# Kernel tuning notes

Hardware: AMD Instinct MI355X
Metric: run time of the kernel (lower is better)

## Reference

```python
import jax, jax.numpy as jnp
import numpy as np

N = 50000   # nodes
E = 600000  # edges
D = 128     # emb_dim
L = 3       # num_layers
G = 500     # graphs in batch
AV = 128    # atom feature vocab per column (9 columns)
BV = 8      # bond feature vocab per column (3 columns)


def setup_inputs() -> dict:
    key = jax.random.key(0)
    ks = jax.random.split(key, 16)
    r = lambda k, sh: jax.random.normal(k, sh, jnp.float32) * 0.02
    return dict(
        x=jax.random.randint(ks[0], (N, 9), 0, AV),
        edge_index=jax.random.randint(ks[1], (2, E), 0, N),
        edge_attr=jax.random.randint(ks[2], (E, 3), 0, BV),
        batch=(jnp.arange(N) * G) // N,  # sorted node->graph map, covers all G graphs
        atom_emb=r(ks[3], (9, AV, D)),
        bond_emb=r(ks[4], (L, 3, BV, D)),  # per-layer BondEncoder
        eps=jnp.zeros((L,), jnp.float32),
        conv_w1=r(ks[5], (L, D, 2 * D)), conv_b1=jnp.zeros((L, 2 * D), jnp.float32),
        conv_bn_g=jnp.ones((L, 2 * D), jnp.float32), conv_bn_b=jnp.zeros((L, 2 * D), jnp.float32),
        conv_w2=r(ks[6], (L, 2 * D, D)), conv_b2=jnp.zeros((L, D), jnp.float32),
        bn_g=jnp.ones((L, D), jnp.float32), bn_b=jnp.zeros((L, D), jnp.float32),
        vn_emb=jnp.zeros((1, D), jnp.float32),  # init constant 0, as in torch code
        vn_w1=r(ks[7], (L - 1, D, 2 * D)), vn_b1=jnp.zeros((L - 1, 2 * D), jnp.float32),
        vn_bn1_g=jnp.ones((L - 1, 2 * D), jnp.float32), vn_bn1_b=jnp.zeros((L - 1, 2 * D), jnp.float32),
        vn_w2=r(ks[8], (L - 1, 2 * D, D)), vn_b2=jnp.zeros((L - 1, D), jnp.float32),
        vn_bn2_g=jnp.ones((L - 1, D), jnp.float32), vn_bn2_b=jnp.zeros((L - 1, D), jnp.float32),
    )


def _bn(h, g, b):
    # BatchNorm1d, training-mode batch statistics (biased var), eps=1e-5
    mu = h.mean(0)
    var = h.var(0)
    return (h - mu) * jax.lax.rsqrt(var + 1e-5) * g + b


def reference(x, edge_index, edge_attr, batch, atom_emb, bond_emb, eps,
              conv_w1, conv_b1, conv_bn_g, conv_bn_b, conv_w2, conv_b2,
              bn_g, bn_b, vn_emb, vn_w1, vn_b1, vn_bn1_g, vn_bn1_b,
              vn_w2, vn_b2, vn_bn2_g, vn_bn2_b):
    src, dst = edge_index[0], edge_index[1]
    # AtomEncoder: sum of per-column embeddings -> [N, D]
    h = sum(atom_emb[i][x[:, i]] for i in range(9))
    vn = jnp.broadcast_to(vn_emb[0], (G, D))  # virtualnode_embedding(zeros(G))
    for l in range(L):
        h = h + vn[batch]                                   # virtual-node broadcast
        ee = sum(bond_emb[l, i][edge_attr[:, i]] for i in range(3))  # BondEncoder [E, D]
        msg = jax.nn.relu(h[src] + ee)                      # message: relu(x_j + edge_attr)
        agg = jax.ops.segment_sum(msg, dst, num_segments=N)  # aggr='add'
        t = (1.0 + eps[l]) * h + agg
        t = _bn(t @ conv_w1[l] + conv_b1[l], conv_bn_g[l], conv_bn_b[l])
        t = jax.nn.relu(t) @ conv_w2[l] + conv_b2[l]
        hn = _bn(t, bn_g[l], bn_b[l])                       # outer batch_norms[layer]
        if l < L - 1:
            hn = jax.nn.relu(hn)                            # relu before dropout (non-final)
            # virtual node update: global_add_pool(h_list[layer]) + vn -> MLP
            vt = jax.ops.segment_sum(h, batch, num_segments=G) + vn
            vt = jax.nn.relu(_bn(vt @ vn_w1[l] + vn_b1[l], vn_bn1_g[l], vn_bn1_b[l]))
            vn = jax.nn.relu(_bn(vt @ vn_w2[l] + vn_b2[l], vn_bn2_g[l], vn_bn2_b[l]))
        h = hn
    return h
```

## Files before the change

kernel.cpp:

```cpp
#include <hip/hip_runtime.h>

#define DEV __global__ __launch_bounds__(256)

constexpr int NN = 50000;
constexpr int NE = 600000;
constexpr int D  = 128;
constexpr int NG = 500;
constexpr int NL = 3;
constexpr int SCAN_B = 512;
constexpr int NBLK = (NN + SCAN_B - 1) / SCAN_B;

typedef __attribute__((ext_vector_type(8))) short bf16x8;
typedef __attribute__((ext_vector_type(4))) float f32x4;

__device__ inline ushort f2bf(float f) {
  unsigned u = __builtin_bit_cast(unsigned, f);
  unsigned r = u + 0x7FFFu + ((u >> 16) & 1u);
  return (ushort)(r >> 16);
}
__device__ inline float bf2f(ushort h) {
  unsigned u = ((unsigned)h) << 16;
  return __builtin_bit_cast(float, u);
}


DEV void k_atom(const int* __restrict__ x, const float* __restrict__ emb,
                const float* __restrict__ vne, float* __restrict__ hv) {
  int t = blockIdx.x * 256 + threadIdx.x;
  int n = t >> 5, c = (t & 31) * 4;
  if (n >= NN) return;
  float4 acc = *(const float4*)(vne + c);
  #pragma unroll
  for (int i = 0; i < 9; ++i) {
    int v = x[n * 9 + i];
    float4 e = *(const float4*)(emb + ((size_t)(i * 128 + v)) * D + c);
    acc.x += e.x; acc.y += e.y; acc.z += e.z; acc.w += e.w;
  }
  *(float4*)(hv + (size_t)n * D + c) = acc;
}

DEV void k_vninit(const float* __restrict__ src, float* __restrict__ vn) {
  int t = blockIdx.x * 256 + threadIdx.x;
  int g = t >> 5, c = (t & 31) * 4;
  if (g >= NG) return;
  *(float4*)(vn + (size_t)g * D + c) = *(const float4*)(src + c);
}

DEV void k_post(const float* __restrict__ z, const float* __restrict__ sum,
                const float* __restrict__ sq, const float* __restrict__ gam,
                const float* __restrict__ bet, float invM,
                const float* __restrict__ vnadd, const int* __restrict__ batch,
                float* __restrict__ dst, int M, int relu) {
  int t = blockIdx.x * 256 + threadIdx.x;
  int n = t >> 5, c = (t & 31) * 4;
  if (n >= M) return;
  f32x4 s = *(const f32x4*)(sum + c);
  f32x4 q = *(const f32x4*)(sq + c);
  f32x4 g = *(const f32x4*)(gam + c);
  f32x4 b = *(const f32x4*)(bet + c);
  f32x4 v = *(const f32x4*)(z + (size_t)n * 128 + c);
  f32x4 o;
  #pragma unroll
  for (int j = 0; j < 4; ++j) {
    float mu = s[j] * invM;
    float var = q[j] * invM - mu * mu;
    float sc = g[j] * rsqrtf(var + 1e-5f);
    float sh = b[j] - mu * sc;
    o[j] = fmaf(v[j], sc, sh);
    if (relu) o[j] = fmaxf(o[j], 0.f);
  }
  if (vnadd) {
    f32x4 a = *(const f32x4*)(vnadd + (size_t)batch[n] * 128 + c);
    #pragma unroll
    for (int j = 0; j < 4; ++j) o[j] += a[j];
  }
  *(f32x4*)(dst + (size_t)n * 128 + c) = o;
}


DEV void k_hist(const int* __restrict__ ei, int* __restrict__ cnt) {
  int e = blockIdx.x * 256 + threadIdx.x;
  if (e < NE) atomicAdd(&cnt[ei[NE + e]], 1);
}

__global__ __launch_bounds__(SCAN_B) void k_scan_a(const int* __restrict__ cnt,
                                                   int* __restrict__ rowptr,
                                                   int* __restrict__ bsum) {
  __shared__ int sh[SCAN_B];
  int i = blockIdx.x * SCAN_B + threadIdx.x;
  int v = (i < NN) ? cnt[i] : 0;
  sh[threadIdx.x] = v;
  __syncthreads();
  for (int off = 1; off < SCAN_B; off <<= 1) {
    int u = (threadIdx.x >= (unsigned)off) ? sh[threadIdx.x - off] : 0;
    __syncthreads();
    sh[threadIdx.x] += u;
    __syncthreads();
  }
  if (i < NN) rowptr[i + 1] = sh[threadIdx.x];
  if (threadIdx.x == SCAN_B - 1) bsum[blockIdx.x] = sh[SCAN_B - 1];
}

__global__ void k_scan_b(int* __restrict__ bsum, int nb) {
  if (threadIdx.x == 0 && blockIdx.x == 0) {
    int acc = 0;
    for (int i = 0; i < nb; ++i) { int v = bsum[i]; bsum[i] = acc; acc += v; }
  }
}

__global__ __launch_bounds__(SCAN_B) void k_scan_c(int* __restrict__ rowptr,
                                                   const int* __restrict__ bsum) {
  int i = blockIdx.x * SCAN_B + threadIdx.x;
  if (i < NN) rowptr[i + 1] += bsum[blockIdx.x];
  if (i == 0) rowptr[0] = 0;
}

DEV void k_fill(const int* __restrict__ ei, const int* __restrict__ eattr,
                int* __restrict__ cursor, unsigned* __restrict__ csr) {
  int e = blockIdx.x * 256 + threadIdx.x;
  if (e >= NE) return;
  int dn = ei[NE + e];
  int p = atomicAdd(&cursor[dn], 1);
  unsigned a0 = (unsigned)eattr[e * 3 + 0];
  unsigned a1 = (unsigned)eattr[e * 3 + 1];
  unsigned a2 = (unsigned)eattr[e * 3 + 2];
  csr[p] = (unsigned)ei[e] | (a0 << 17) | (a1 << 20) | (a2 << 23);
}


DEV void k_agg(const float* __restrict__ hv, const unsigned* __restrict__ csr,
               const int* __restrict__ rowptr, const float* __restrict__ bond,
               float* __restrict__ agg) {
  __shared__ float eb[3 * 8 * D];
  for (int i = threadIdx.x; i < 3 * 8 * D; i += 256) eb[i] = bond[i];
  __syncthreads();
  int wid = (blockIdx.x * 256 + threadIdx.x) >> 6;
  int lane = threadIdx.x & 63;
  if (wid >= NN) return;
  int d0 = lane * 2;
  float ax = 0.f, ay = 0.f;
  int p = rowptr[wid];
  const int p1 = rowptr[wid + 1];
  for (; p + 4 <= p1; p += 4) {
    unsigned pk[4];
    #pragma unroll
    for (int j = 0; j < 4; ++j) pk[j] = csr[p + j];
    float2 hvv[4];
    #pragma unroll
    for (int j = 0; j < 4; ++j)
      hvv[j] = *(const float2*)(hv + (size_t)(pk[j] & 0x1FFFF) * D + d0);
    #pragma unroll
    for (int j = 0; j < 4; ++j) {
      float2 e0 = *(const float2*)(eb + (((pk[j] >> 17) & 7u)) * D + d0);
      float2 e1 = *(const float2*)(eb + (8 + ((pk[j] >> 20) & 7u)) * D + d0);
      float2 e2 = *(const float2*)(eb + (16 + ((pk[j] >> 23) & 7u)) * D + d0);
      ax += fmaxf(hvv[j].x + e0.x + e1.x + e2.x, 0.f);
      ay += fmaxf(hvv[j].y + e0.y + e1.y + e2.y, 0.f);
    }
  }
  for (; p < p1; ++p) {
    unsigned pk = csr[p];
    float2 hvv = *(const float2*)(hv + (size_t)(pk & 0x1FFFF) * D + d0);
    float2 e0 = *(const float2*)(eb + (((pk >> 17) & 7u)) * D + d0);
    float2 e1 = *(const float2*)(eb + (8 + ((pk >> 20) & 7u)) * D + d0);
    float2 e2 = *(const float2*)(eb + (16 + ((pk >> 23) & 7u)) * D + d0);
    ax += fmaxf(hvv.x + e0.x + e1.x + e2.x, 0.f);
    ay += fmaxf(hvv.y + e0.y + e1.y + e2.y, 0.f);
  }
  *(float2*)(agg + (size_t)wid * D + d0) = make_float2(ax, ay);
}

__global__ __launch_bounds__(256) void k_cvtw(const float* __restrict__ src, int K,
                                              int lognc, ushort* __restrict__ th,
                                              ushort* __restrict__ tl) {
  int NC = 1 << lognc;
  size_t base = (size_t)blockIdx.y * K * NC;
  int i = blockIdx.x * 256 + threadIdx.x;
  if (i >= K * NC) return;
  int k = i >> lognc, c = i & (NC - 1);
  float v = src[base + i];
  ushort hi = f2bf(v);
  th[base + (size_t)c * K + k] = hi;
  tl[base + (size_t)c * K + k] = f2bf(v - bf2f(hi));
}

template <int AMODE, int COLS, int NT>
__global__ __launch_bounds__(NT) void k_mgemm(
    int M, int K, const float* __restrict__ A0, const float* __restrict__ A1,
    const float* __restrict__ epsp, const float* __restrict__ bnsum,
    const float* __restrict__ bnsq, const float* __restrict__ bngam,
    const float* __restrict__ bnbet, float invPrevM,
    const ushort* __restrict__ Wth, const ushort* __restrict__ Wtl,
    const float* __restrict__ bias, float* __restrict__ Y,
    float* __restrict__ colsum, float* __restrict__ colsq) {
  constexpr int NWC = COLS / 64;
  __shared__ __align__(16) ushort Ah[4][128][8];
  __shared__ __align__(16) ushort Al[4][128][8];
  __shared__ __align__(16) ushort Bh[4][COLS][8];
  __shared__ __align__(16) ushort Bl[4][COLS][8];
  __shared__ float bnsc[AMODE == 2 ? 256 : 1];
  __shared__ float bnsh[AMODE == 2 ? 256 : 1];
  const int tid = threadIdx.x;
  const int row0 = blockIdx.x * 128;
  const int lane = tid & 63, w = tid >> 6;
  const int wr = w / NWC, wc = w % NWC;
  const int kc = lane >> 4, lr = lane & 15;

  if (AMODE == 2) {
    for (int c = tid; c < K; c += NT) {
      float mu = bnsum[c] * invPrevM;
      float var = bnsq[c] * invPrevM - mu * mu;
      float sc = bngam[c] * rsqrtf(var + 1e-5f);
      bnsc[c] = sc;
      bnsh[c] = bnbet[c] - mu * sc;
    }
    __syncthreads();
  }

  float ef = 0.f;
  if (AMODE == 1) ef = 1.f + *epsp;
  f32x4 acc[4][4] = {};

  for (int k0 = 0; k0 < K; k0 += 32) {
    for (int i = tid; i < 512; i += NT) {
      const int c = i >> 7, r = i & 127;
      const int gk = k0 + c * 8;
      const int gr = row0 + r;
      float v[8];
      if (gr < M) {
        f32x4 a0 = *(const f32x4*)(A0 + (size_t)gr * K + gk);
        f32x4 a1 = *(const f32x4*)(A0 + (size_t)gr * K + gk + 4);
        if (AMODE == 1) {
          f32x4 g0 = *(const f32x4*)(A1 + (size_t)gr * K + gk);
          f32x4 g1 = *(const f32x4*)(A1 + (size_t)gr * K + gk + 4);
          #pragma unroll
          for (int j = 0; j < 4; ++j) {
            v[j] = fmaf(ef, a0[j], g0[j]);
            v[4 + j] = fmaf(ef, a1[j], g1[j]);
          }
        } else if (AMODE == 2) {
          f32x4 s0 = *(const f32x4*)&bnsc[gk];
          f32x4 s1 = *(const f32x4*)&bnsc[gk + 4];
          f32x4 t0 = *(const f32x4*)&bnsh[gk];
          f32x4 t1 = *(const f32x4*)&bnsh[gk + 4];
          #pragma unroll
          for (int j = 0; j < 4; ++j) {
            v[j] = fmaxf(fmaf(a0[j], s0[j], t0[j]), 0.f);
            v[4 + j] = fmaxf(fmaf(a1[j], s1[j], t1[j]), 0.f);
          }
        } else {
          #pragma unroll
          for (int j = 0; j < 4; ++j) { v[j] = a0[j]; v[4 + j] = a1[j]; }
        }
      } else {
        #pragma unroll
        for (int j = 0; j < 8; ++j) v[j] = 0.f;
      }
      alignas(16) ushort th[8], tl[8];
      #pragma unroll
      for (int j = 0; j < 8; ++j) {
        ushort hi = f2bf(v[j]);
        th[j] = hi;
        tl[j] = f2bf(v[j] - bf2f(hi));
      }
      *(uint4*)&Ah[c][r][0] = *(const uint4*)th;
      *(uint4*)&Al[c][r][0] = *(const uint4*)tl;
    }
    for (int i = tid; i < COLS * 4; i += NT) {
      const int c = i / COLS, r = i % COLS;
      const int gk = k0 + c * 8;
      *(uint4*)&Bh[c][r][0] = *(const uint4*)(Wth + (size_t)r * K + gk);
      *(uint4*)&Bl[c][r][0] = *(const uint4*)(Wtl + (size_t)r * K + gk);
    }
    __syncthreads();
    bf16x8 bhf[4], blf[4];
    #pragma unroll
    for (int fc = 0; fc < 4; ++fc) {
      bhf[fc] = *(const bf16x8*)&Bh[kc][wc * 64 + fc * 16 + lr][0];
      blf[fc] = *(const bf16x8*)&Bl[kc][wc * 64 + fc * 16 + lr][0];
    }
    #pragma unroll
    for (int fr = 0; fr < 4; ++fr) {
      bf16x8 ahf = *(const bf16x8*)&Ah[kc][wr * 64 + fr * 16 + lr][0];
      bf16x8 alf = *(const bf16x8*)&Al[kc][wr * 64 + fr * 16 + lr][0];
      #pragma unroll
      for (int fc = 0; fc < 4; ++fc) {
        acc[fr][fc] = __builtin_amdgcn_mfma_f32_16x16x32_bf16(ahf, bhf[fc], acc[fr][fc], 0, 0, 0);
        acc[fr][fc] = __builtin_amdgcn_mfma_f32_16x16x32_bf16(alf, bhf[fc], acc[fr][fc], 0, 0, 0);
        acc[fr][fc] = __builtin_amdgcn_mfma_f32_16x16x32_bf16(ahf, blf[fc], acc[fr][fc], 0, 0, 0);
      }
    }
    __syncthreads();
  }

  #pragma unroll
  for (int fc = 0; fc < 4; ++fc) {
    const int gc = wc * 64 + fc * 16 + lr;
    const float bb = bias[gc];
    float cs = 0.f, cq = 0.f;
    #pragma unroll
    for (int fr = 0; fr < 4; ++fr) {
      const int rb = row0 + wr * 64 + fr * 16 + kc * 4;
      #pragma unroll
      for (int rg = 0; rg < 4; ++rg) {
        int gr = rb + rg;
        if (gr < M) {
          float v = acc[fr][fc][rg] + bb;
          Y[(size_t)gr * COLS + gc] = v;
          cs += v;
          cq += v * v;
        }
      }
    }
    cs += __shfl_xor(cs, 16); cs += __shfl_xor(cs, 32);
    cq += __shfl_xor(cq, 16); cq += __shfl_xor(cq, 32);
    if (kc == 0) {
      atomicAdd(&colsum[gc], cs);
      atomicAdd(&colsq[gc], cq);
    }
  }
}


DEV void k_pool(const float* __restrict__ hv, const int* __restrict__ batch,
                const float* __restrict__ vn, float* __restrict__ vt) {
  int g = blockIdx.x;
  int lo = 0, hi = NN;
  while (lo < hi) { int mid = (lo + hi) >> 1; if (batch[mid] < g) lo = mid + 1; else hi = mid; }
  int s = lo;
  hi = NN;
  while (lo < hi) { int mid = (lo + hi) >> 1; if (batch[mid] < g + 1) lo = mid + 1; else hi = mid; }
  int e = lo;
  int ry = threadIdx.x >> 5, cx = threadIdx.x & 31;
  float4 acc = make_float4(0.f, 0.f, 0.f, 0.f);
  for (int n = s + ry; n < e; n += 8) {
    float4 v = *(const float4*)(hv + (size_t)n * D + cx * 4);
    acc.x += v.x; acc.y += v.y; acc.z += v.z; acc.w += v.w;
  }
  __shared__ float4 red[8][32];
  red[ry][cx] = acc;
  __syncthreads();
  for (int st = 4; st >= 1; st >>= 1) {
    if (ry < st) {
      float4 o = red[ry + st][cx];
      red[ry][cx].x += o.x; red[ry][cx].y += o.y;
      red[ry][cx].z += o.z; red[ry][cx].w += o.w;
    }
    __syncthreads();
  }
  if (ry == 0) {
    float4 v = red[0][cx];
    float4 b = *(const float4*)(vn + (size_t)g * D + cx * 4);
    v.x += b.x; v.y += b.y; v.z += b.z; v.w += b.w;
    *(float4*)(vt + (size_t)g * D + cx * 4) = v;
  }
}


extern "C" void kernel_launch(void* const* d_in, const int* in_sizes, int n_in,
                              void* d_out, int out_size, void* d_ws, size_t ws_size,
                              hipStream_t stream) {
  const int* x = (const int*)d_in[0];
  const int* ei = (const int*)d_in[1];
  const int* eattr = (const int*)d_in[2];
  const int* batch = (const int*)d_in[3];
  const float* atom_emb = (const float*)d_in[4];
  const float* bond_emb = (const float*)d_in[5];
  const float* eps = (const float*)d_in[6];
  const float* conv_w1 = (const float*)d_in[7];
  const float* conv_b1 = (const float*)d_in[8];
  const float* conv_bn_g = (const float*)d_in[9];
  const float* conv_bn_b = (const float*)d_in[10];
  const float* conv_w2 = (const float*)d_in[11];
  const float* conv_b2 = (const float*)d_in[12];
  const float* bn_g = (const float*)d_in[13];
  const float* bn_b = (const float*)d_in[14];
  const float* vn_emb = (const float*)d_in[15];
  const float* vn_w1 = (const float*)d_in[16];
  const float* vn_b1 = (const float*)d_in[17];
  const float* vn_bn1_g = (const float*)d_in[18];
  const float* vn_bn1_b = (const float*)d_in[19];
  const float* vn_w2 = (const float*)d_in[20];
  const float* vn_b2 = (const float*)d_in[21];
  const float* vn_bn2_g = (const float*)d_in[22];
  const float* vn_bn2_b = (const float*)d_in[23];
  float* out = (float*)d_out;

  char* w = (char*)d_ws;
  auto alloc = [&](size_t bytes) {
    char* p = w;
    w += (bytes + 255) & ~((size_t)255);
    return p;
  };
  float* h   = (float*)alloc((size_t)NN * D * 4);
  float* hv  = (float*)alloc((size_t)NN * D * 4);
  float* agg = (float*)alloc((size_t)NN * D * 4);
  float* y   = (float*)alloc((size_t)NN * 256 * 4);
  float* vn  = (float*)alloc((size_t)NG * D * 4);
  float* vt  = (float*)alloc((size_t)NG * D * 4);
  float* yv  = (float*)alloc((size_t)NG * 256 * 4);
  float* zv  = (float*)alloc((size_t)NG * D * 4);
  float* stats = (float*)alloc(16 * 512 * 4);
  auto SUM = [&](int slot) { return stats + slot * 512; };
  auto SQ  = [&](int slot) { return stats + slot * 512 + 256; };
  int* cnt = (int*)alloc((size_t)NN * 4);
  int* rowptr = (int*)alloc((size_t)(NN + 1) * 4);
  int* cursor = (int*)alloc((size_t)NN * 4);
  unsigned* csr = (unsigned*)alloc((size_t)NE * 4);
  int* bsum = (int*)alloc(128 * 4);
  ushort* wt1h = (ushort*)alloc((size_t)NL * 256 * 128 * 2);
  ushort* wt1l = (ushort*)alloc((size_t)NL * 256 * 128 * 2);
  ushort* wt2h = (ushort*)alloc((size_t)NL * 128 * 256 * 2);
  ushort* wt2l = (ushort*)alloc((size_t)NL * 128 * 256 * 2);
  ushort* vw1h = (ushort*)alloc((size_t)2 * 256 * 128 * 2);
  ushort* vw1l = (ushort*)alloc((size_t)2 * 256 * 128 * 2);
  ushort* vw2h = (ushort*)alloc((size_t)2 * 128 * 256 * 2);
  ushort* vw2l = (ushort*)alloc((size_t)2 * 128 * 256 * 2);

  hipMemsetAsync(stats, 0, 16 * 512 * 4, stream);

  k_cvtw<<<dim3(128, NL), 256, 0, stream>>>(conv_w1, 128, 8, wt1h, wt1l);
  k_cvtw<<<dim3(128, NL), 256, 0, stream>>>(conv_w2, 256, 7, wt2h, wt2l);
  k_cvtw<<<dim3(128, 2), 256, 0, stream>>>(vn_w1, 128, 8, vw1h, vw1l);
  k_cvtw<<<dim3(128, 2), 256, 0, stream>>>(vn_w2, 256, 7, vw2h, vw2l);

  k_atom<<<(NN * 32 + 255) / 256, 256, 0, stream>>>(x, atom_emb, vn_emb, hv);
  k_vninit<<<(NG * 32 + 255) / 256, 256, 0, stream>>>(vn_emb, vn);

  hipMemsetAsync(cnt, 0, (size_t)NN * 4, stream);
  k_hist<<<(NE + 255) / 256, 256, 0, stream>>>(ei, cnt);
  k_scan_a<<<NBLK, SCAN_B, 0, stream>>>(cnt, rowptr, bsum);
  k_scan_b<<<1, 64, 0, stream>>>(bsum, NBLK);
  k_scan_c<<<NBLK, SCAN_B, 0, stream>>>(rowptr, bsum);
  hipMemcpyAsync(cursor, rowptr, (size_t)NN * 4, hipMemcpyDeviceToDevice, stream);
  k_fill<<<(NE + 255) / 256, 256, 0, stream>>>(ei, eattr, cursor, csr);

  const int gx = (NN + 127) / 128;
  const int gv = (NG + 127) / 128;
  for (int l = 0; l < NL; ++l) {
    const int sc1 = l, sc2 = 3 + l, sv1 = 6 + l, sv2 = 8 + l;
    k_agg<<<(NN * 64 + 255) / 256, 256, 0, stream>>>(
        hv, csr, rowptr, bond_emb + (size_t)l * 3 * 8 * D, agg);

    k_mgemm<1, 256, 512><<<gx, 512, 0, stream>>>(
        NN, 128, hv, agg, eps + l, nullptr, nullptr, nullptr, nullptr, 0.f,
        wt1h + (size_t)l * 256 * 128, wt1l + (size_t)l * 256 * 128,
        conv_b1 + l * 256, y, SUM(sc1), SQ(sc1));
    k_mgemm<2, 128, 256><<<gx, 256, 0, stream>>>(
        NN, 256, y, nullptr, nullptr, SUM(sc1), SQ(sc1),
        conv_bn_g + l * 256, conv_bn_b + l * 256, 1.f / NN,
        wt2h + (size_t)l * 128 * 256, wt2l + (size_t)l * 128 * 256,
        conv_b2 + l * 128, h, SUM(sc2), SQ(sc2));

    if (l < NL - 1) {
      k_pool<<<NG, 256, 0, stream>>>(hv, batch, vn, vt);
      k_mgemm<0, 256, 512><<<gv, 512, 0, stream>>>(
          NG, 128, vt, nullptr, nullptr, nullptr, nullptr, nullptr, nullptr, 0.f,
          vw1h + (size_t)l * 256 * 128, vw1l + (size_t)l * 256 * 128,
          vn_b1 + l * 256, yv, SUM(sv1), SQ(sv1));
      k_mgemm<2, 128, 256><<<gv, 256, 0, stream>>>(
          NG, 256, yv, nullptr, nullptr, SUM(sv1), SQ(sv1),
          vn_bn1_g + l * 256, vn_bn1_b + l * 256, 1.f / NG,
          vw2h + (size_t)l * 128 * 256, vw2l + (size_t)l * 128 * 256,
          vn_b2 + l * 128, zv, SUM(sv2), SQ(sv2));
      k_post<<<(NG * 32 + 255) / 256, 256, 0, stream>>>(
          zv, SUM(sv2), SQ(sv2), vn_bn2_g + l * 128, vn_bn2_b + l * 128,
          1.f / NG, nullptr, nullptr, vn, NG, 1);
      k_post<<<(NN * 32 + 255) / 256, 256, 0, stream>>>(
          h, SUM(sc2), SQ(sc2), bn_g + l * 128, bn_b + l * 128,
          1.f / NN, vn, batch, hv, NN, 1);
    } else {
      k_post<<<(NN * 32 + 255) / 256, 256, 0, stream>>>(
          h, SUM(sc2), SQ(sc2), bn_g + l * 128, bn_b + l * 128,
          1.f / NN, nullptr, nullptr, out, NN, 0);
    }
  }
}
```

Before: 874.8 us.

## Fuse eps-combine and bf16 split into aggregation; replace stat atomics with block partials

The aggregation kernel now adds (1+eps)*h itself and writes the result pre-split into bf16 hi/lo arrays. The first GEMM loads these directly instead of reading two fp32 tensors and converting them. Column sum and sum-of-squares for batch norm are first reduced across waves in shared memory. For the large GEMMs each block then writes per-block partials that a small reduction kernel sums, replacing global atomics. This cuts GEMM input traffic and atomic contention, at the cost of two extra kernel launches per layer and a serial loop over about 391 blocks in the reduction.

```diff
diff --git a/kernel.cpp b/kernel.cpp
--- a/kernel.cpp
+++ b/kernel.cpp
@@ -130,7 +130,8 @@
 
 DEV void k_agg(const float* __restrict__ hv, const unsigned* __restrict__ csr,
                const int* __restrict__ rowptr, const float* __restrict__ bond,
-               float* __restrict__ agg) {
+               const float* __restrict__ epsp, unsigned* __restrict__ Ahi,
+               unsigned* __restrict__ Alo) {
   __shared__ float eb[3 * 8 * D];
   for (int i = threadIdx.x; i < 3 * 8 * D; i += 256) eb[i] = bond[i];
   __syncthreads();
@@ -167,7 +168,14 @@
     ax += fmaxf(hvv.x + e0.x + e1.x + e2.x, 0.f);
     ay += fmaxf(hvv.y + e0.y + e1.y + e2.y, 0.f);
   }
-  *(float2*)(agg + (size_t)wid * D + d0) = make_float2(ax, ay);
+  float2 hvo = *(const float2*)(hv + (size_t)wid * D + d0);
+  float ef = 1.f + epsp[0];
+  float a0 = fmaf(ef, hvo.x, ax);
+  float a1 = fmaf(ef, hvo.y, ay);
+  ushort h0 = f2bf(a0), h1 = f2bf(a1);
+  ushort l0 = f2bf(a0 - bf2f(h0)), l1 = f2bf(a1 - bf2f(h1));
+  Ahi[(size_t)wid * 64 + lane] = (unsigned)h0 | ((unsigned)h1 << 16);
+  Alo[(size_t)wid * 64 + lane] = (unsigned)l0 | ((unsigned)l1 << 16);
 }
 
 __global__ __launch_bounds__(256) void k_cvtw(const float* __restrict__ src, int K,
@@ -184,15 +192,16 @@
   tl[base + (size_t)c * K + k] = f2bf(v - bf2f(hi));
 }
 
-template <int AMODE, int COLS, int NT>
+template <int AMODE, int COLS, int NT, bool ATOMIC>
 __global__ __launch_bounds__(NT) void k_mgemm(
-    int M, int K, const float* __restrict__ A0, const float* __restrict__ A1,
-    const float* __restrict__ epsp, const float* __restrict__ bnsum,
+    int M, int K, const float* __restrict__ A0, const ushort* __restrict__ Ath,
+    const ushort* __restrict__ Atl, const float* __restrict__ bnsum,
     const float* __restrict__ bnsq, const float* __restrict__ bngam,
     const float* __restrict__ bnbet, float invPrevM,
     const ushort* __restrict__ Wth, const ushort* __restrict__ Wtl,
     const float* __restrict__ bias, float* __restrict__ Y,
-    float* __restrict__ colsum, float* __restrict__ colsq) {
+    float* __restrict__ colsum, float* __restrict__ colsq,
+    float* __restrict__ partial) {
   constexpr int NWC = COLS / 64;
   __shared__ __align__(16) ushort Ah[4][128][8];
   __shared__ __align__(16) ushort Al[4][128][8];
@@ -217,8 +226,6 @@
     __syncthreads();
   }
 
-  float ef = 0.f;
-  if (AMODE == 1) ef = 1.f + *epsp;
   f32x4 acc[4][4] = {};
 
   for (int k0 = 0; k0 < K; k0 += 32) {
@@ -226,45 +233,47 @@
       const int c = i >> 7, r = i & 127;
       const int gk = k0 + c * 8;
       const int gr = row0 + r;
-      float v[8];
-      if (gr < M) {
-        f32x4 a0 = *(const f32x4*)(A0 + (size_t)gr * K + gk);
-        f32x4 a1 = *(const f32x4*)(A0 + (size_t)gr * K + gk + 4);
-        if (AMODE == 1) {
-          f32x4 g0 = *(const f32x4*)(A1 + (size_t)gr * K + gk);
-          f32x4 g1 = *(const f32x4*)(A1 + (size_t)gr * K + gk + 4);
-          #pragma unroll
-          for (int j = 0; j < 4; ++j) {
-            v[j] = fmaf(ef, a0[j], g0[j]);
-            v[4 + j] = fmaf(ef, a1[j], g1[j]);
-          }
-        } else if (AMODE == 2) {
-          f32x4 s0 = *(const f32x4*)&bnsc[gk];
-          f32x4 s1 = *(const f32x4*)&bnsc[gk + 4];
-          f32x4 t0 = *(const f32x4*)&bnsh[gk];
-          f32x4 t1 = *(const f32x4*)&bnsh[gk + 4];
-          #pragma unroll
-          for (int j = 0; j < 4; ++j) {
-            v[j] = fmaxf(fmaf(a0[j], s0[j], t0[j]), 0.f);
-            v[4 + j] = fmaxf(fmaf(a1[j], s1[j], t1[j]), 0.f);
+      if (AMODE == 3) {
+        uint4 vh = make_uint4(0, 0, 0, 0), vl = make_uint4(0, 0, 0, 0);
+        if (gr < M) {
+          vh = *(const uint4*)(Ath + (size_t)gr * K + gk);
+          vl = *(const uint4*)(Atl + (size_t)gr * K + gk);
+        }
+        *(uint4*)&Ah[c][r][0] = vh;
+        *(uint4*)&Al[c][r][0] = vl;
+      } else {
+        float v[8];
+        if (gr < M) {
+          f32x4 a0 = *(const f32x4*)(A0 + (size_t)gr * K + gk);
+          f32x4 a1 = *(const f32x4*)(A0 + (size_t)gr * K + gk + 4);
+          if (AMODE == 2) {
+            f32x4 s0 = *(const f32x4*)&bnsc[gk];
+            f32x4 s1 = *(const f32x4*)&bnsc[gk + 4];
+            f32x4 t0 = *(const f32x4*)&bnsh[gk];
+            f32x4 t1 = *(const f32x4*)&bnsh[gk + 4];
+            #pragma unroll
+            for (int j = 0; j < 4; ++j) {
+              v[j] = fmaxf(fmaf(a0[j], s0[j], t0[j]), 0.f);
+              v[4 + j] = fmaxf(fmaf(a1[j], s1[j], t1[j]), 0.f);
+            }
+          } else {
+            #pragma unroll
+            for (int j = 0; j < 4; ++j) { v[j] = a0[j]; v[4 + j] = a1[j]; }
           }
         } else {
           #pragma unroll
-          for (int j = 0; j < 4; ++j) { v[j] = a0[j]; v[4 + j] = a1[j]; }
+          for (int j = 0; j < 8; ++j) v[j] = 0.f;
         }
-      } else {
+        alignas(16) ushort th[8], tl[8];
         #pragma unroll
-        for (int j = 0; j < 8; ++j) v[j] = 0.f;
+        for (int j = 0; j < 8; ++j) {
+          ushort hi = f2bf(v[j]);
+          th[j] = hi;
+          tl[j] = f2bf(v[j] - bf2f(hi));
+        }
+        *(uint4*)&Ah[c][r][0] = *(const uint4*)th;
+        *(uint4*)&Al[c][r][0] = *(const uint4*)tl;
       }
-      alignas(16) ushort th[8], tl[8];
-      #pragma unroll
-      for (int j = 0; j < 8; ++j) {
-        ushort hi = f2bf(v[j]);
-        th[j] = hi;
-        tl[j] = f2bf(v[j] - bf2f(hi));
-      }
-      *(uint4*)&Ah[c][r][0] = *(const uint4*)th;
-      *(uint4*)&Al[c][r][0] = *(const uint4*)tl;
     }
     for (int i = tid; i < COLS * 4; i += NT) {
       const int c = i / COLS, r = i % COLS;
@@ -293,6 +302,8 @@
     __syncthreads();
   }
 
+  float* sred = reinterpret_cast<float*>(&Ah[0][0][0]);
+  float* qred = sred + 2 * COLS;
   #pragma unroll
   for (int fc = 0; fc < 4; ++fc) {
     const int gc = wc * 64 + fc * 16 + lr;
@@ -315,10 +326,33 @@
     cs += __shfl_xor(cs, 16); cs += __shfl_xor(cs, 32);
     cq += __shfl_xor(cq, 16); cq += __shfl_xor(cq, 32);
     if (kc == 0) {
-      atomicAdd(&colsum[gc], cs);
-      atomicAdd(&colsq[gc], cq);
-    }
-  }
+      sred[wr * COLS + gc] = cs;
+      qred[wr * COLS + gc] = cq;
+    }
+  }
+  __syncthreads();
+  for (int c = tid; c < COLS; c += NT) {
+    float s = sred[c] + sred[COLS + c];
+    float q = qred[c] + qred[COLS + c];
+    if (ATOMIC) {
+      atomicAdd(&colsum[c], s);
+      atomicAdd(&colsq[c], q);
+    } else {
+      partial[(size_t)blockIdx.x * 2 * COLS + c] = s;
+      partial[(size_t)blockIdx.x * 2 * COLS + COLS + c] = q;
+    }
+  }
+}
+
+__global__ __launch_bounds__(256) void k_red(const float* __restrict__ part, int nb,
+                                             int width, float* __restrict__ outSum,
+                                             float* __restrict__ outSq) {
+  int j = blockIdx.x * 256 + threadIdx.x;
+  if (j >= 2 * width) return;
+  float a = 0.f;
+  for (int b = 0; b < nb; ++b) a += part[(size_t)b * 2 * width + j];
+  if (j < width) outSum[j] = a;
+  else outSq[j - width] = a;
 }
 
 
@@ -394,8 +428,9 @@
   };
   float* h   = (float*)alloc((size_t)NN * D * 4);
   float* hv  = (float*)alloc((size_t)NN * D * 4);
-  float* agg = (float*)alloc((size_t)NN * D * 4);
   float* y   = (float*)alloc((size_t)NN * 256 * 4);
+  unsigned* Ahi = (unsigned*)alloc((size_t)NN * 64 * 4);
+  unsigned* Alo = (unsigned*)alloc((size_t)NN * 64 * 4);
   float* vn  = (float*)alloc((size_t)NG * D * 4);
   float* vt  = (float*)alloc((size_t)NG * D * 4);
   float* yv  = (float*)alloc((size_t)NG * 256 * 4);
@@ -403,6 +438,10 @@
   float* stats = (float*)alloc(16 * 512 * 4);
   auto SUM = [&](int slot) { return stats + slot * 512; };
   auto SQ  = [&](int slot) { return stats + slot * 512 + 256; };
+  const int gx = (NN + 127) / 128;
+  const int gv = (NG + 127) / 128;
+  float* partA = (float*)alloc((size_t)gx * 512 * 4);
+  float* partB = (float*)alloc((size_t)gx * 256 * 4);
   int* cnt = (int*)alloc((size_t)NN * 4);
   int* rowptr = (int*)alloc((size_t)(NN + 1) * 4);
   int* cursor = (int*)alloc((size_t)NN * 4);
@@ -435,34 +474,35 @@
   hipMemcpyAsync(cursor, rowptr, (size_t)NN * 4, hipMemcpyDeviceToDevice, stream);
   k_fill<<<(NE + 255) / 256, 256, 0, stream>>>(ei, eattr, cursor, csr);
 
-  const int gx = (NN + 127) / 128;
-  const int gv = (NG + 127) / 128;
   for (int l = 0; l < NL; ++l) {
     const int sc1 = l, sc2 = 3 + l, sv1 = 6 + l, sv2 = 8 + l;
     k_agg<<<(NN * 64 + 255) / 256, 256, 0, stream>>>(
-        hv, csr, rowptr, bond_emb + (size_t)l * 3 * 8 * D, agg);
-
-    k_mgemm<1, 256, 512><<<gx, 512, 0, stream>>>(
-        NN, 128, hv, agg, eps + l, nullptr, nullptr, nullptr, nullptr, 0.f,
+        hv, csr, rowptr, bond_emb + (size_t)l * 3 * 8 * D, eps + l, Ahi, Alo);
+
+    k_mgemm<3, 256, 512, false><<<gx, 512, 0, stream>>>(
+        NN, 128, nullptr, (const ushort*)Ahi, (const ushort*)Alo,
+        nullptr, nullptr, nullptr, nullptr, 0.f,
         wt1h + (size_t)l * 256 * 128, wt1l + (size_t)l * 256 * 128,
-        conv_b1 + l * 256, y, SUM(sc1), SQ(sc1));
-    k_mgemm<2, 128, 256><<<gx, 256, 0, stream>>>(
+        conv_b1 + l * 256, y, nullptr, nullptr, partA);
+    k_red<<<2, 256, 0, stream>>>(partA, gx, 256, SUM(sc1), SQ(sc1));
+    k_mgemm<2, 128, 256, false><<<gx, 256, 0, stream>>>(
         NN, 256, y, nullptr, nullptr, SUM(sc1), SQ(sc1),
         conv_bn_g + l * 256, conv_bn_b + l * 256, 1.f / NN,
         wt2h + (size_t)l * 128 * 256, wt2l + (size_t)l * 128 * 256,
-        conv_b2 + l * 128, h, SUM(sc2), SQ(sc2));
+        conv_b2 + l * 128, h, nullptr, nullptr, partB);
+    k_red<<<1, 256, 0, stream>>>(partB, gx, 128, SUM(sc2), SQ(sc2));
 
     if (l < NL - 1) {
       k_pool<<<NG, 256, 0, stream>>>(hv, batch, vn, vt);
-      k_mgemm<0, 256, 512><<<gv, 512, 0, stream>>>(
+      k_mgemm<0, 256, 512, true><<<gv, 512, 0, stream>>>(
           NG, 128, vt, nullptr, nullptr, nullptr, nullptr, nullptr, nullptr, 0.f,
           vw1h + (size_t)l * 256 * 128, vw1l + (size_t)l * 256 * 128,
-          vn_b1 + l * 256, yv, SUM(sv1), SQ(sv1));
-      k_mgemm<2, 128, 256><<<gv, 256, 0, stream>>>(
+          vn_b1 + l * 256, yv, SUM(sv1), SQ(sv1), nullptr);
+      k_mgemm<2, 128, 256, true><<<gv, 256, 0, stream>>>(
           NG, 256, yv, nullptr, nullptr, SUM(sv1), SQ(sv1),
           vn_bn1_g + l * 256, vn_bn1_b + l * 256, 1.f / NG,
           vw2h + (size_t)l * 128 * 256, vw2l + (size_t)l * 128 * 256,
-          vn_b2 + l * 128, zv, SUM(sv2), SQ(sv2));
+          vn_b2 + l * 128, zv, SUM(sv2), SQ(sv2), nullptr);
       k_post<<<(NG * 32 + 255) / 256, 256, 0, stream>>>(
           zv, SUM(sv2), SQ(sv2), vn_bn2_g + l * 128, vn_bn2_b + l * 128,
           1.f / NG, nullptr, nullptr, vn, NG, 1);
```

Result: slower. 1.377 ms (+57.4%).
